# Kernel optimization log

Hardware: AMD Instinct MI355X
Metric: run time of the kernel (lower is better)

Reference implementation:

```python
import jax, jax.numpy as jnp
import numpy as np

B, L, D, H = 8, 1024, 1024, 16
DH = D // H  # dim_per_head = 64
HG = H // 2  # global/local head split


def setup_inputs() -> dict:
    key = jax.random.key(0)
    ks = jax.random.split(key, 10)
    s = 1.0 / np.sqrt(D)
    return {
        "key": jax.random.normal(ks[0], (B, L, D), jnp.float32),
        "value": jax.random.normal(ks[1], (B, L, D), jnp.float32),
        "query": jax.random.normal(ks[2], (B, L, D), jnp.float32),
        "mask": jax.random.bernoulli(ks[3], 0.1, (B, L, L)),
        "additional_mask": jax.random.bernoulli(ks[4], 0.1, (B, L)),
        "Wk": jax.random.normal(ks[5], (D, D), jnp.float32) * s,
        "bk": jnp.zeros((D,), jnp.float32),
        "Wv": jax.random.normal(ks[6], (D, D), jnp.float32) * s,
        "bv": jnp.zeros((D,), jnp.float32),
        "Wq": jax.random.normal(ks[7], (D, D), jnp.float32) * s,
        "bq": jnp.zeros((D,), jnp.float32),
        "Wo": jax.random.normal(ks[8], (D, D), jnp.float32) * s,
        "bo": jnp.zeros((D,), jnp.float32),
    }


def _shape(x):
    # [B, L, D] -> [B, H, L, DH]
    return x.reshape(B, -1, H, DH).transpose(0, 2, 1, 3)


def reference(key, value, query, mask, additional_mask,
              Wk, bk, Wv, bv, Wq, bq, Wo, bo):
    # projections (torch Linear: x @ W.T + b)
    k = _shape(key @ Wk.T + bk)
    v = _shape(value @ Wv.T + bv)
    q = _shape(query @ Wq.T + bq) * (1.0 / np.sqrt(DH))  # scale query (edge_feature=None, additional_mask given)

    qg, ql = q[:, :HG], q[:, HG:]
    kg, kl = k[:, :HG], k[:, HG:]
    vg, vl = v[:, :HG], v[:, HG:]

    # global heads: standard masked attention
    score_g = jnp.einsum('bhqd,bhkd->bhqk', qg, kg)
    top_score = score_g[:, 0]  # taken BEFORE masking, as in original
    score_g = jnp.where(mask[:, None, :, :], -1e18, score_g)
    attn_g = jax.nn.softmax(score_g, axis=-1)  # dropout = identity (eval)
    ctx_g = jnp.einsum('bhqk,bhkd->bhqd', attn_g, vg)

    # local heads: additional_mask [B, k] broadcast over heads and queries
    score_l = jnp.einsum('bhqd,bhkd->bhqk', ql, kl)
    score_l = jnp.where(additional_mask[:, None, None, :], -1e18, score_l)
    attn_l = jax.nn.softmax(score_l, axis=-1)
    ctx_l = jnp.einsum('bhqk,bhkd->bhqd', attn_l, vl)

    ctx = jnp.concatenate([ctx_g, ctx_l], axis=1)          # [B, H, L, DH]
    ctx = ctx.transpose(0, 2, 1, 3).reshape(B, -1, D)      # unshape -> [B, L, D]
    out = ctx @ Wo.T + bo
    return out, top_score
```

## Files before the change

kernel.cpp:

```cpp
#include <hip/hip_runtime.h>
#include <hip/hip_bf16.h>

typedef unsigned short u16;
typedef unsigned int u32;
typedef __attribute__((ext_vector_type(8))) short short8;
typedef __attribute__((ext_vector_type(4))) short short4v;
typedef __attribute__((ext_vector_type(4))) float floatx4;

#define BB 8
#define LL 1024
#define DD 1024
#define HH 16
#define DHH 64
#define NEGBIG (-3.0e38f)
#define QSCALE 0.1803368801111204f
#define LN2F   0.6931471805599453f

__device__ inline u16 f2b(float f) {
  union { __hip_bfloat16 h; u16 u; } cv;
  cv.h = __float2bfloat16(f);
  return cv.u;
}
__device__ inline float b2f(u16 u) {
  union { u16 u; __hip_bfloat16 h; } cv;
  cv.u = u;
  return __bfloat162float(cv.h);
}
__device__ inline float fin(float v, float sentinel) {
  return (fabsf(v) < 1e30f) ? v : sentinel;
}
__device__ inline float fexp2(float x) {
#if __has_builtin(__builtin_amdgcn_exp2f)
  return __builtin_amdgcn_exp2f(x);
#else
  return exp2f(x);
#endif
}
__device__ inline void async16(const void* g, void* l) {
  __builtin_amdgcn_global_load_lds(
      (__attribute__((address_space(1))) void*)(const_cast<void*>(g)),
      (__attribute__((address_space(3))) void*)l, 16, 0, 0);
}


__global__ __launch_bounds__(256) void convpack(
    const float* __restrict__ key, const float* __restrict__ value,
    const float* __restrict__ Wk, const float* __restrict__ Wv,
    const float* __restrict__ Wq, const float* __restrict__ Wo,
    const int* __restrict__ mask, const int* __restrict__ amask,
    u16* __restrict__ keyb, u16* __restrict__ valb, u16* __restrict__ Wkb,
    u16* __restrict__ Wvb, u16* __restrict__ Wqb, u16* __restrict__ Wob,
    u32* __restrict__ maskb, u32* __restrict__ amaskb) {
  const int job = blockIdx.y;
  const int gtid = blockIdx.x * 256 + threadIdx.x;
  const int stride = gridDim.x * 256;

  if (job < 6) {
    const float* src; u16* dst; size_t n4;
    switch (job) {
      case 0: src = key;   dst = keyb; n4 = (size_t)BB * LL * DD / 4; break;
      case 1: src = value; dst = valb; n4 = (size_t)BB * LL * DD / 4; break;
      case 2: src = Wk;    dst = Wkb;  n4 = (size_t)DD * DD / 4; break;
      case 3: src = Wv;    dst = Wvb;  n4 = (size_t)DD * DD / 4; break;
      case 4: src = Wq;    dst = Wqb;  n4 = (size_t)DD * DD / 4; break;
      default: src = Wo;   dst = Wob;  n4 = (size_t)DD * DD / 4; break;
    }
    for (size_t i = gtid; i < n4; i += stride) {
      float4 v = ((const float4*)src)[i];
      short4v s;
      s[0] = (short)f2b(v.x); s[1] = (short)f2b(v.y);
      s[2] = (short)f2b(v.z); s[3] = (short)f2b(v.w);
      *(short4v*)(dst + i * 4) = s;
    }
  } else if (job == 6) {
    const size_t nw = (size_t)BB * LL * LL / 32;
    for (size_t w = gtid; w < nw; w += stride) {
      const int4* src = (const int4*)(mask + w * 32);
      u32 bits = 0;
#pragma unroll
      for (int c = 0; c < 8; c++) {
        int4 v = src[c];
        bits |= (u32)(v.x != 0) << (c * 4);
        bits |= (u32)(v.y != 0) << (c * 4 + 1);
        bits |= (u32)(v.z != 0) << (c * 4 + 2);
        bits |= (u32)(v.w != 0) << (c * 4 + 3);
      }
      maskb[w] = bits;
    }
  } else {
    const int nw = BB * LL / 32;
    for (int w = gtid; w < nw; w += stride) {
      const int4* src = (const int4*)(amask + w * 32);
      u32 bits = 0;
#pragma unroll
      for (int c = 0; c < 8; c++) {
        int4 v = src[c];
        bits |= (u32)(v.x != 0) << (c * 4);
        bits |= (u32)(v.y != 0) << (c * 4 + 1);
        bits |= (u32)(v.z != 0) << (c * 4 + 2);
        bits |= (u32)(v.w != 0) << (c * 4 + 3);
      }
      amaskb[w] = bits;
    }
  }
}

__global__ __launch_bounds__(256) void gemm_qkv(
    const u16* __restrict__ keyb, const u16* __restrict__ valb,
    const float* __restrict__ query, const u16* __restrict__ Wkb,
    const u16* __restrict__ Wvb, const u16* __restrict__ Wqb,
    const float* __restrict__ bk, const float* __restrict__ bv,
    const float* __restrict__ bq, u16* __restrict__ kbuf,
    u16* __restrict__ vbt, u16* __restrict__ qbuf) {
  __shared__ u16 As[128 * 32];
  __shared__ u16 Ws[128 * 32];

  const int z = blockIdx.z;
  const int tid = threadIdx.x;
  const int wave = tid >> 6, lane = tid & 63;
  const int lr = lane & 15, lq = lane >> 4;
  const int row0 = blockIdx.x * 128;
  const int col0 = blockIdx.y * 128;
  const int wm = (wave & 1) * 64, wn = (wave >> 1) * 64;

  floatx4 acc[4][4];
#pragma unroll
  for (int i = 0; i < 4; i++)
#pragma unroll
    for (int j = 0; j < 4; j++) acc[i][j] = (floatx4){0.f, 0.f, 0.f, 0.f};

  const int cc0 = tid, cc1 = 256 + tid;
  u16* As0 = As + wave * 512;
  u16* As1 = As + 2048 + wave * 512;
  u16* Ws0 = Ws + wave * 512;
  u16* Ws1 = Ws + 2048 + wave * 512;

  if (z < 2) {
    const u16* A  = (z == 0) ? keyb : valb;
    const u16* Wb = (z == 0) ? Wkb : Wvb;
    const u16* Ag0 = A + (size_t)(row0 + (cc0 >> 2)) * 1024 + (cc0 & 3) * 8;
    const u16* Ag1 = A + (size_t)(row0 + (cc1 >> 2)) * 1024 + (cc1 & 3) * 8;
    const u16* Wg0 = Wb + (size_t)(col0 + (cc0 >> 2)) * 1024 + (cc0 & 3) * 8;
    const u16* Wg1 = Wb + (size_t)(col0 + (cc1 >> 2)) * 1024 + (cc1 & 3) * 8;

    for (int k0 = 0; k0 < 1024; k0 += 32) {
      __syncthreads();
      async16(Ag0 + k0, As0);
      async16(Ag1 + k0, As1);
      async16(Wg0 + k0, Ws0);
      async16(Wg1 + k0, Ws1);
      __syncthreads();

      short8 af[4], wf[4];
#pragma unroll
      for (int mi = 0; mi < 4; mi++)
        af[mi] = *(const short8*)(As + (wm + mi * 16 + lr) * 32 + lq * 8);
#pragma unroll
      for (int ni = 0; ni < 4; ni++)
        wf[ni] = *(const short8*)(Ws + (wn + ni * 16 + lr) * 32 + lq * 8);
#pragma unroll
      for (int mi = 0; mi < 4; mi++)
#pragma unroll
        for (int ni = 0; ni < 4; ni++)
          acc[mi][ni] = __builtin_amdgcn_mfma_f32_16x16x32_bf16(af[mi], wf[ni],
                                                                acc[mi][ni], 0, 0, 0);
    }
  } else {
    const u16* Wg0 = Wqb + (size_t)(col0 + (cc0 >> 2)) * 1024 + (cc0 & 3) * 8;
    const u16* Wg1 = Wqb + (size_t)(col0 + (cc1 >> 2)) * 1024 + (cc1 & 3) * 8;

    for (int k0 = 0; k0 < 1024; k0 += 32) {
      float4 ag[4];
#pragma unroll
      for (int it = 0; it < 4; it++) {
        const int cc = it * 256 + tid;
        ag[it] = *(const float4*)(query + (size_t)(row0 + (cc >> 3)) * 1024 +
                                  (cc & 7) * 4 + k0);
      }
      __syncthreads();
      async16(Wg0 + k0, Ws0);
      async16(Wg1 + k0, Ws1);
#pragma unroll
      for (int it = 0; it < 4; it++) {
        const int cc = it * 256 + tid;
        short4v s;
        s[0] = (short)f2b(ag[it].x); s[1] = (short)f2b(ag[it].y);
        s[2] = (short)f2b(ag[it].z); s[3] = (short)f2b(ag[it].w);
        *(short4v*)(As + (cc >> 3) * 32 + (cc & 7) * 4) = s;
      }
      __syncthreads();

      short8 af[4], wf[4];
#pragma unroll
      for (int mi = 0; mi < 4; mi++)
        af[mi] = *(const short8*)(As + (wm + mi * 16 + lr) * 32 + lq * 8);
#pragma unroll
      for (int ni = 0; ni < 4; ni++)
        wf[ni] = *(const short8*)(Ws + (wn + ni * 16 + lr) * 32 + lq * 8);
#pragma unroll
      for (int mi = 0; mi < 4; mi++)
#pragma unroll
        for (int ni = 0; ni < 4; ni++)
          acc[mi][ni] = __builtin_amdgcn_mfma_f32_16x16x32_bf16(af[mi], wf[ni],
                                                                acc[mi][ni], 0, 0, 0);
    }
  }

  const float scale = (z == 2) ? QSCALE : 1.0f;
  const float* bias = (z == 0) ? bk : (z == 1) ? bv : bq;
  u16* outb = (z == 0) ? kbuf : qbuf;

#pragma unroll
  for (int ni = 0; ni < 4; ni++) {
    const int col = col0 + wn + ni * 16 + lr;
    const float bvv = bias[col];
#pragma unroll
    for (int mi = 0; mi < 4; mi++) {
#pragma unroll
      for (int r = 0; r < 4; r++) {
        const int row = row0 + wm + mi * 16 + lq * 4 + r;
        const float v = (acc[mi][ni][r] + bvv) * scale;
        const int b = row >> 10, l = row & 1023, h = col >> 6, dh = col & 63;
        if (z == 1)
          vbt[((b * HH + h) * DHH + dh) * LL + l] = f2b(v);
        else
          outb[((b * HH + h) * LL + l) * DHH + dh] = f2b(v);
      }
    }
  }
}

template <int OUT>
__global__ __launch_bounds__(256) void gemm_b(
    const u16* __restrict__ A, const u16* __restrict__ Wb,
    const float* __restrict__ bias, void* __restrict__ outv, float scale) {
  __shared__ u16 As[128 * 32];
  __shared__ u16 Ws[128 * 32];

  const int tid = threadIdx.x;
  const int wave = tid >> 6, lane = tid & 63;
  const int lr = lane & 15, lq = lane >> 4;
  const int row0 = blockIdx.x * 128;
  const int col0 = blockIdx.y * 128;
  const int wm = (wave & 1) * 64, wn = (wave >> 1) * 64;

  floatx4 acc[4][4];
#pragma unroll
  for (int i = 0; i < 4; i++)
#pragma unroll
    for (int j = 0; j < 4; j++) acc[i][j] = (floatx4){0.f, 0.f, 0.f, 0.f};

  const int cc0 = tid, cc1 = 256 + tid;
  const u16* Ag0 = A + (size_t)(row0 + (cc0 >> 2)) * 1024 + (cc0 & 3) * 8;
  const u16* Ag1 = A + (size_t)(row0 + (cc1 >> 2)) * 1024 + (cc1 & 3) * 8;
  const u16* Wg0 = Wb + (size_t)(col0 + (cc0 >> 2)) * 1024 + (cc0 & 3) * 8;
  const u16* Wg1 = Wb + (size_t)(col0 + (cc1 >> 2)) * 1024 + (cc1 & 3) * 8;
  u16* As0 = As + wave * 512;
  u16* As1 = As + 2048 + wave * 512;
  u16* Ws0 = Ws + wave * 512;
  u16* Ws1 = Ws + 2048 + wave * 512;

  for (int k0 = 0; k0 < 1024; k0 += 32) {
    __syncthreads();
    async16(Ag0 + k0, As0);
    async16(Ag1 + k0, As1);
    async16(Wg0 + k0, Ws0);
    async16(Wg1 + k0, Ws1);
    __syncthreads();

    short8 af[4], wf[4];
#pragma unroll
    for (int mi = 0; mi < 4; mi++)
      af[mi] = *(const short8*)(As + (wm + mi * 16 + lr) * 32 + lq * 8);
#pragma unroll
    for (int ni = 0; ni < 4; ni++)
      wf[ni] = *(const short8*)(Ws + (wn + ni * 16 + lr) * 32 + lq * 8);
#pragma unroll
    for (int mi = 0; mi < 4; mi++)
#pragma unroll
      for (int ni = 0; ni < 4; ni++)
        acc[mi][ni] = __builtin_amdgcn_mfma_f32_16x16x32_bf16(af[mi], wf[ni],
                                                              acc[mi][ni], 0, 0, 0);
  }

#pragma unroll
  for (int ni = 0; ni < 4; ni++) {
    const int col = col0 + wn + ni * 16 + lr;
    const float bv = bias[col];
#pragma unroll
    for (int mi = 0; mi < 4; mi++) {
#pragma unroll
      for (int r = 0; r < 4; r++) {
        const int row = row0 + wm + mi * 16 + lq * 4 + r;
        const float v = (acc[mi][ni][r] + bv) * scale;
        if (OUT == 0) {
          const int b = row >> 10, l = row & 1023, h = col >> 6, dh = col & 63;
          ((u16*)outv)[((b * HH + h) * LL + l) * DHH + dh] = f2b(v);
        } else if (OUT == 2) {
          const int b = row >> 10, l = row & 1023, h = col >> 6, dh = col & 63;
          ((u16*)outv)[((b * HH + h) * DHH + dh) * LL + l] = f2b(v);
        } else {
          ((float*)outv)[(size_t)row * 1024 + col] = v;
        }
      }
    }
  }
}

__global__ __launch_bounds__(256) void attn_fast(
    const u16* __restrict__ qbuf, const u16* __restrict__ kbuf,
    const u16* __restrict__ vbt, const u32* __restrict__ maskb,
    const u32* __restrict__ amaskb, u16* __restrict__ ctx,
    float* __restrict__ top) {
  __shared__ u16 Ks[2][64 * 64];
  __shared__ u16 Vts[2][64 * 64];

  const int id = blockIdx.x;
  const int xcd = id & 7;
  const int r_ = id >> 3;
  const int b = r_ & 7;
  const int h = (((r_ >> 3) & 1) << 3) | (xcd ^ b);
  const int qt = r_ >> 4;

  const int tid = threadIdx.x, wave = tid >> 6, lane = tid & 63;
  const int lr = lane & 15, lq = lane >> 4;
  const int lq4 = lq * 4;
  const int x7 = lr & 7;

  const u16* Qg = qbuf + (size_t)((b * HH + h) * LL + qt * 128) * DHH;
  const u16* Kg = kbuf + (size_t)((b * HH + h) * LL) * DHH;
  const u16* Vtg = vbt + (size_t)((b * HH + h) * DHH) * LL;

  short8 qf[2][2];
#pragma unroll
  for (int mi = 0; mi < 2; mi++)
#pragma unroll
    for (int kk = 0; kk < 2; kk++)
      qf[mi][kk] = *(const short8*)(Qg + (wave * 32 + mi * 16 + lr) * 64 +
                                    kk * 32 + lq * 8);

  const int g0 = tid, g1 = 256 + tid;
  const int kr0 = g0 >> 3, kc0 = (g0 & 7) ^ (kr0 & 7);
  const int kr1 = g1 >> 3, kc1 = (g1 & 7) ^ (kr1 & 7);
  const int cs0 = ((0 + lq) ^ x7) * 8;
  const int cs1 = ((4 + lq) ^ x7) * 8;
  const int lqh = lq >> 1, lqb = (lq & 1) * 4;
  const int go00 = ((0 + lqh) ^ x7) * 8 + lqb;
  const int go01 = ((2 + lqh) ^ x7) * 8 + lqb;
  const int go10 = ((4 + lqh) ^ x7) * 8 + lqb;
  const int go11 = ((6 + lqh) ^ x7) * 8 + lqb;

  auto stage = [&](int kc, int buf) {
    async16(Kg + kc * 4096 + kr0 * 64 + kc0 * 8, &Ks[buf][wave * 512]);
    async16(Kg + kc * 4096 + kr1 * 64 + kc1 * 8, &Ks[buf][2048 + wave * 512]);
    async16(Vtg + (size_t)kr0 * LL + kc * 64 + kc0 * 8, &Vts[buf][wave * 512]);
    async16(Vtg + (size_t)kr1 * LL + kc * 64 + kc1 * 8,
            &Vts[buf][2048 + wave * 512]);
  };

  float mrow[2], lrow[2];
  floatx4 Oacc[2][4];
#pragma unroll
  for (int mi = 0; mi < 2; mi++) {
    mrow[mi] = NEGBIG;
    lrow[mi] = 0.f;
#pragma unroll
    for (int ni = 0; ni < 4; ni++) Oacc[mi][ni] = (floatx4){0.f, 0.f, 0.f, 0.f};
  }

  stage(0, 0);

  for (int kc = 0; kc < 16; kc++) {
    const int cur = kc & 1;
    __syncthreads();
    if (kc < 15) stage(kc + 1, cur ^ 1);
    const u16* Ksc = Ks[cur];
    const u16* Vtsc = Vts[cur];

    floatx4 S[2][4];
    __builtin_amdgcn_s_setprio(1);
#pragma unroll
    for (int nj = 0; nj < 4; nj++) {
      const short8 kf0 = *(const short8*)(Ksc + (nj * 16 + lr) * 64 + cs0);
      const short8 kf1 = *(const short8*)(Ksc + (nj * 16 + lr) * 64 + cs1);
#pragma unroll
      for (int mi = 0; mi < 2; mi++) {
        floatx4 z = (floatx4){0.f, 0.f, 0.f, 0.f};
        z = __builtin_amdgcn_mfma_f32_16x16x32_bf16(kf1, qf[mi][1], z, 0, 0, 0);
        z = __builtin_amdgcn_mfma_f32_16x16x32_bf16(kf0, qf[mi][0], z, 0, 0, 0);
        S[mi][nj] = z;
      }
    }
    __builtin_amdgcn_s_setprio(0);

    short8 pf[2][2];
#pragma unroll
    for (int mi = 0; mi < 2; mi++) {
      const int row = qt * 128 + wave * 32 + mi * 16 + lr;

      if (h == 0) {
        float* tp = top + (size_t)(b * LL + row) * LL + kc * 64 + lq4;
#pragma unroll
        for (int nj = 0; nj < 4; nj++) {
          float4 t;
          t.x = S[mi][nj][0] * LN2F; t.y = S[mi][nj][1] * LN2F;
          t.z = S[mi][nj][2] * LN2F; t.w = S[mi][nj][3] * LN2F;
          *(float4*)(tp + nj * 16) = t;
        }
      }

      if (h < 8) {
        const uint2 mw =
            *(const uint2*)(maskb + (size_t)(b * LL + row) * 32 + kc * 2);
#pragma unroll
        for (int nj = 0; nj < 4; nj++) {
          const u32 nib = (((nj & 2) ? mw.y : mw.x) >> ((nj & 1) * 16 + lq4)) & 15u;
#pragma unroll
          for (int r = 0; r < 4; r++)
            if ((nib >> r) & 1) S[mi][nj][r] = -1e18f;
        }
      } else {
        const uint2 aw = *(const uint2*)(amaskb + b * 32 + kc * 2);
#pragma unroll
        for (int nj = 0; nj < 4; nj++) {
          const u32 nib = (((nj & 2) ? aw.y : aw.x) >> ((nj & 1) * 16 + lq4)) & 15u;
#pragma unroll
          for (int r = 0; r < 4; r++)
            if ((nib >> r) & 1) S[mi][nj][r] = -1e18f;
        }
      }

      float cm = fmaxf(fmaxf(S[mi][0][0], S[mi][0][1]),
                       fmaxf(S[mi][0][2], S[mi][0][3]));
#pragma unroll
      for (int nj = 1; nj < 4; nj++)
        cm = fmaxf(cm, fmaxf(fmaxf(S[mi][nj][0], S[mi][nj][1]),
                             fmaxf(S[mi][nj][2], S[mi][nj][3])));
      cm = fmaxf(cm, __shfl_xor(cm, 16, 64));
      cm = fmaxf(cm, __shfl_xor(cm, 32, 64));
      const float mold = mrow[mi];
      const float mnew = fmaxf(mold, cm);
      const float alpha = fexp2(mold - mnew);
      mrow[mi] = mnew;
      float rs = 0.f;
#pragma unroll
      for (int nj = 0; nj < 4; nj++)
#pragma unroll
        for (int r = 0; r < 4; r++) {
          const float p = fexp2(S[mi][nj][r] - mnew);
          S[mi][nj][r] = p;
          rs += p;
        }
      rs += __shfl_xor(rs, 16, 64);
      rs += __shfl_xor(rs, 32, 64);
      lrow[mi] = lrow[mi] * alpha + rs;
#pragma unroll
      for (int ni = 0; ni < 4; ni++)
#pragma unroll
        for (int r = 0; r < 4; r++) Oacc[mi][ni][r] *= alpha;

#pragma unroll
      for (int kk = 0; kk < 2; kk++) {
        short8 p;
#pragma unroll
        for (int r = 0; r < 4; r++) {
          p[r] = (short)f2b(S[mi][2 * kk][r]);
          p[4 + r] = (short)f2b(S[mi][2 * kk + 1][r]);
        }
        pf[mi][kk] = p;
      }
    }

    __builtin_amdgcn_s_setprio(1);
#pragma unroll
    for (int ni = 0; ni < 4; ni++) {
      const int rb = (ni * 16 + lr) * 64;
      const short4v v00 = *(const short4v*)(Vtsc + rb + go00);
      const short4v v01 = *(const short4v*)(Vtsc + rb + go01);
      const short4v v10 = *(const short4v*)(Vtsc + rb + go10);
      const short4v v11 = *(const short4v*)(Vtsc + rb + go11);
      const short8 vf0 = __builtin_shufflevector(v00, v01, 0, 1, 2, 3, 4, 5, 6, 7);
      const short8 vf1 = __builtin_shufflevector(v10, v11, 0, 1, 2, 3, 4, 5, 6, 7);
#pragma unroll
      for (int mi = 0; mi < 2; mi++) {
        Oacc[mi][ni] =
            __builtin_amdgcn_mfma_f32_16x16x32_bf16(vf0, pf[mi][0], Oacc[mi][ni], 0, 0, 0);
        Oacc[mi][ni] =
            __builtin_amdgcn_mfma_f32_16x16x32_bf16(vf1, pf[mi][1], Oacc[mi][ni], 0, 0, 0);
      }
    }
    __builtin_amdgcn_s_setprio(0);
  }

#pragma unroll
  for (int mi = 0; mi < 2; mi++) {
    const float inv = 1.0f / lrow[mi];
    const int row = qt * 128 + wave * 32 + mi * 16 + lr;
    u16* cp = ctx + (size_t)(b * LL + row) * DD + h * DHH + lq4;
#pragma unroll
    for (int ni = 0; ni < 4; ni++) {
      short4v o;
      o[0] = (short)f2b(Oacc[mi][ni][0] * inv);
      o[1] = (short)f2b(Oacc[mi][ni][1] * inv);
      o[2] = (short)f2b(Oacc[mi][ni][2] * inv);
      o[3] = (short)f2b(Oacc[mi][ni][3] * inv);
      *(short4v*)(cp + ni * 16) = o;
    }
  }
}

template <int MODE>
__global__ __launch_bounds__(256) void gemm_k(
    const void* __restrict__ Av, const float* __restrict__ W,
    const float* __restrict__ biasp, void* __restrict__ outv, float scale) {
  __shared__ u16 As[128 * 32];
  __shared__ u16 Ws[128 * 32];
  const int tid = threadIdx.x;
  const int wave = tid >> 6, lane = tid & 63;
  const int lr = lane & 15, lq = lane >> 4;
  const int row0 = blockIdx.x * 128;
  const int col0 = blockIdx.y * 128;
  const int wm = (wave & 1) * 64, wn = (wave >> 1) * 64;
  floatx4 acc[4][4];
#pragma unroll
  for (int i = 0; i < 4; i++)
#pragma unroll
    for (int j = 0; j < 4; j++) acc[i][j] = (floatx4){0.f, 0.f, 0.f, 0.f};
  const float* Af = (const float*)Av;
  const u16* Ab = (const u16*)Av;
  for (int k0 = 0; k0 < 1024; k0 += 32) {
    float4 wg[4];
#pragma unroll
    for (int it = 0; it < 4; it++) {
      const int cc = it * 256 + tid;
      wg[it] = *(const float4*)(W + (size_t)(col0 + (cc >> 3)) * 1024 + (cc & 7) * 4 + k0);
    }
    float4 ag[4];
    short8 ab0, ab1;
    if (MODE == 0) {
#pragma unroll
      for (int it = 0; it < 4; it++) {
        const int cc = it * 256 + tid;
        ag[it] = *(const float4*)(Af + (size_t)(row0 + (cc >> 3)) * 1024 + (cc & 7) * 4 + k0);
      }
    } else {
      const int cc0 = tid, cc1 = 256 + tid;
      ab0 = *(const short8*)(Ab + (size_t)(row0 + (cc0 >> 2)) * 1024 + (cc0 & 3) * 8 + k0);
      ab1 = *(const short8*)(Ab + (size_t)(row0 + (cc1 >> 2)) * 1024 + (cc1 & 3) * 8 + k0);
    }
    __syncthreads();
#pragma unroll
    for (int it = 0; it < 4; it++) {
      const int cc = it * 256 + tid;
      short4v s;
      s[0] = (short)f2b(wg[it].x); s[1] = (short)f2b(wg[it].y);
      s[2] = (short)f2b(wg[it].z); s[3] = (short)f2b(wg[it].w);
      *(short4v*)(Ws + (cc >> 3) * 32 + (cc & 7) * 4) = s;
    }
    if (MODE == 0) {
#pragma unroll
      for (int it = 0; it < 4; it++) {
        const int cc = it * 256 + tid;
        short4v s;
        s[0] = (short)f2b(ag[it].x); s[1] = (short)f2b(ag[it].y);
        s[2] = (short)f2b(ag[it].z); s[3] = (short)f2b(ag[it].w);
        *(short4v*)(As + (cc >> 3) * 32 + (cc & 7) * 4) = s;
      }
    } else {
      *(short8*)(As + tid * 8) = ab0;
      *(short8*)(As + (256 + tid) * 8) = ab1;
    }
    __syncthreads();
    short8 af[4], wf[4];
#pragma unroll
    for (int mi = 0; mi < 4; mi++)
      af[mi] = *(const short8*)(As + (wm + mi * 16 + lr) * 32 + lq * 8);
#pragma unroll
    for (int ni = 0; ni < 4; ni++)
      wf[ni] = *(const short8*)(Ws + (wn + ni * 16 + lr) * 32 + lq * 8);
#pragma unroll
    for (int mi = 0; mi < 4; mi++)
#pragma unroll
      for (int ni = 0; ni < 4; ni++)
        acc[mi][ni] = __builtin_amdgcn_mfma_f32_16x16x32_bf16(af[mi], wf[ni], acc[mi][ni], 0, 0, 0);
  }
#pragma unroll
  for (int ni = 0; ni < 4; ni++) {
    const int col = col0 + wn + ni * 16 + lr;
    const float bv = biasp[col];
#pragma unroll
    for (int mi = 0; mi < 4; mi++) {
#pragma unroll
      for (int r = 0; r < 4; r++) {
        const int row = row0 + wm + mi * 16 + lq * 4 + r;
        float v = (acc[mi][ni][r] + bv) * scale;
        v = fin(v, MODE == 0 ? 700.0f : 1000.0f);
        if (MODE == 0) {
          const int b = row >> 10, l = row & 1023, h = col >> 6, dh = col & 63;
          ((u16*)outv)[((b * HH + h) * LL + l) * DHH + dh] = f2b(v);
        } else {
          ((float*)outv)[(size_t)row * 1024 + col] = v;
        }
      }
    }
  }
}

__global__ __launch_bounds__(256) void attn_kernel(
    const u16* __restrict__ qbuf, const u16* __restrict__ kbuf,
    const u16* __restrict__ vbuf, const int* __restrict__ mask,
    const int* __restrict__ amask, u16* __restrict__ ctx,
    float* __restrict__ top) {
  __shared__ u16 Qs[128 * 64];
  __shared__ u16 Ks[64 * 64];
  __shared__ u16 Vts[64 * 64];
  __shared__ u16 Ps[4][32 * 64];
  const int qt = blockIdx.x, h = blockIdx.y, b = blockIdx.z;
  const int tid = threadIdx.x, wave = tid >> 6, lane = tid & 63;
  const int lr = lane & 15, lq = lane >> 4;
  const u16* Qg = qbuf + (size_t)((b * HH + h) * LL + qt * 128) * DHH;
  const u16* Kg = kbuf + (size_t)((b * HH + h) * LL) * DHH;
  const u16* Vg = vbuf + (size_t)((b * HH + h) * LL) * DHH;
#pragma unroll
  for (int it = 0; it < 4; it++) {
    short8 qv = *(const short8*)(Qg + (it * 256 + tid) * 8);
    *(short8*)(Qs + (it * 256 + tid) * 8) = qv;
  }
  float mrow[2][4], lrow[2][4];
  floatx4 Oacc[2][4];
#pragma unroll
  for (int mi = 0; mi < 2; mi++)
#pragma unroll
    for (int r = 0; r < 4; r++) { mrow[mi][r] = NEGBIG; lrow[mi][r] = 0.f; }
#pragma unroll
  for (int mi = 0; mi < 2; mi++)
#pragma unroll
    for (int ni = 0; ni < 4; ni++) Oacc[mi][ni] = (floatx4){0.f, 0.f, 0.f, 0.f};
  for (int kc = 0; kc < 16; kc++) {
    const u16* Kc = Kg + kc * 64 * DHH;
    const u16* Vc = Vg + kc * 64 * DHH;
    short8 kv0 = *(const short8*)(Kc + tid * 8);
    short8 kv1 = *(const short8*)(Kc + (256 + tid) * 8);
    short8 vv0 = *(const short8*)(Vc + tid * 8);
    short8 vv1 = *(const short8*)(Vc + (256 + tid) * 8);
    __syncthreads();
    *(short8*)(Ks + tid * 8) = kv0;
    *(short8*)(Ks + (256 + tid) * 8) = kv1;
    {
      const int r0 = tid >> 3, e0 = (tid & 7) * 8;
#pragma unroll
      for (int j = 0; j < 8; j++) Vts[(e0 + j) * 64 + r0] = (u16)vv0[j];
      const int cc1 = 256 + tid;
      const int r1 = cc1 >> 3, e1 = (cc1 & 7) * 8;
#pragma unroll
      for (int j = 0; j < 8; j++) Vts[(e1 + j) * 64 + r1] = (u16)vv1[j];
    }
    __syncthreads();
    floatx4 S[2][4];
    short8 qf[2][2];
#pragma unroll
    for (int mi = 0; mi < 2; mi++)
#pragma unroll
      for (int kk = 0; kk < 2; kk++)
        qf[mi][kk] = *(const short8*)(Qs + (wave * 32 + mi * 16 + lr) * 64 + kk * 32 + lq * 8);
#pragma unroll
    for (int nj = 0; nj < 4; nj++) {
      short8 kf0 = *(const short8*)(Ks + (nj * 16 + lr) * 64 + lq * 8);
      short8 kf1 = *(const short8*)(Ks + (nj * 16 + lr) * 64 + 32 + lq * 8);
#pragma unroll
      for (int mi = 0; mi < 2; mi++) {
        floatx4 z = (floatx4){0.f, 0.f, 0.f, 0.f};
        z = __builtin_amdgcn_mfma_f32_16x16x32_bf16(qf[mi][1], kf1, z, 0, 0, 0);
        z = __builtin_amdgcn_mfma_f32_16x16x32_bf16(qf[mi][0], kf0, z, 0, 0, 0);
        S[mi][nj] = z;
      }
    }
#pragma unroll
    for (int mi = 0; mi < 2; mi++)
#pragma unroll
      for (int nj = 0; nj < 4; nj++)
#pragma unroll
        for (int r = 0; r < 4; r++) S[mi][nj][r] = fin(S[mi][nj][r], 800.0f);
    if (h == 0) {
#pragma unroll
      for (int mi = 0; mi < 2; mi++)
#pragma unroll
        for (int nj = 0; nj < 4; nj++)
#pragma unroll
          for (int r = 0; r < 4; r++) {
            const int row = qt * 128 + wave * 32 + mi * 16 + lq * 4 + r;
            const int colk = kc * 64 + nj * 16 + lr;
            top[(size_t)(b * LL + row) * LL + colk] = S[mi][nj][r];
          }
    }
    if (h < 8) {
#pragma unroll
      for (int mi = 0; mi < 2; mi++)
#pragma unroll
        for (int r = 0; r < 4; r++) {
          const int row = qt * 128 + wave * 32 + mi * 16 + lq * 4 + r;
          const int* mp = mask + (size_t)(b * LL + row) * LL + kc * 64;
#pragma unroll
          for (int nj = 0; nj < 4; nj++) {
            const int mv = mp[nj * 16 + lr];
            S[mi][nj][r] = mv ? -1e18f : S[mi][nj][r];
          }
        }
    } else {
#pragma unroll
      for (int nj = 0; nj < 4; nj++) {
        const int mv = amask[b * LL + kc * 64 + nj * 16 + lr];
        if (mv) {
#pragma unroll
          for (int mi = 0; mi < 2; mi++)
#pragma unroll
            for (int r = 0; r < 4; r++) S[mi][nj][r] = -1e18f;
        }
      }
    }
#pragma unroll
    for (int mi = 0; mi < 2; mi++) {
#pragma unroll
      for (int r = 0; r < 4; r++) {
        float cm = S[mi][0][r];
#pragma unroll
        for (int nj = 1; nj < 4; nj++) cm = fmaxf(cm, S[mi][nj][r]);
#pragma unroll
        for (int off = 1; off < 16; off <<= 1) cm = fmaxf(cm, __shfl_xor(cm, off, 64));
        const float mold = mrow[mi][r];
        const float mnew = fmaxf(mold, cm);
        const float alpha = __expf(mold - mnew);
        mrow[mi][r] = mnew;
        float rs = 0.f;
#pragma unroll
        for (int nj = 0; nj < 4; nj++) {
          const float p = __expf(S[mi][nj][r] - mnew);
          S[mi][nj][r] = p;
          rs += p;
        }
#pragma unroll
        for (int off = 1; off < 16; off <<= 1) rs += __shfl_xor(rs, off, 64);
        lrow[mi][r] = lrow[mi][r] * alpha + rs;
#pragma unroll
        for (int ni = 0; ni < 4; ni++) Oacc[mi][ni][r] *= alpha;
      }
    }
#pragma unroll
    for (int mi = 0; mi < 2; mi++)
#pragma unroll
      for (int nj = 0; nj < 4; nj++)
#pragma unroll
        for (int r = 0; r < 4; r++)
          Ps[wave][(mi * 16 + lq * 4 + r) * 64 + nj * 16 + lr] = f2b(S[mi][nj][r]);
    __syncthreads();
#pragma unroll
    for (int kk = 0; kk < 2; kk++) {
      short8 pf[2];
#pragma unroll
      for (int mi = 0; mi < 2; mi++)
        pf[mi] = *(const short8*)(&Ps[wave][(mi * 16 + lr) * 64 + kk * 32 + lq * 8]);
#pragma unroll
      for (int ni = 0; ni < 4; ni++) {
        short8 vf = *(const short8*)(Vts + (ni * 16 + lr) * 64 + kk * 32 + lq * 8);
#pragma unroll
        for (int mi = 0; mi < 2; mi++)
          Oacc[mi][ni] = __builtin_amdgcn_mfma_f32_16x16x32_bf16(pf[mi], vf, Oacc[mi][ni], 0, 0, 0);
      }
    }
  }
#pragma unroll
  for (int mi = 0; mi < 2; mi++)
#pragma unroll
    for (int r = 0; r < 4; r++) {
      const float inv = 1.0f / lrow[mi][r];
      const int row = qt * 128 + wave * 32 + mi * 16 + lq * 4 + r;
#pragma unroll
      for (int ni = 0; ni < 4; ni++) {
        const int col = h * DHH + ni * 16 + lr;
        ctx[(size_t)(b * LL + row) * DD + col] = f2b(fin(Oacc[mi][ni][r] * inv, 900.0f));
      }
    }
}

extern "C" void kernel_launch(void* const* d_in, const int* in_sizes, int n_in,
                              void* d_out, int out_size, void* d_ws, size_t ws_size,
                              hipStream_t stream) {
  const float* key   = (const float*)d_in[0];
  const float* value = (const float*)d_in[1];
  const float* query = (const float*)d_in[2];
  const int* mask    = (const int*)d_in[3];
  const int* amask   = (const int*)d_in[4];
  const float* Wk = (const float*)d_in[5];
  const float* bk = (const float*)d_in[6];
  const float* Wv = (const float*)d_in[7];
  const float* bv = (const float*)d_in[8];
  const float* Wq = (const float*)d_in[9];
  const float* bq = (const float*)d_in[10];
  const float* Wo = (const float*)d_in[11];
  const float* bo = (const float*)d_in[12];

  float* outp = (float*)d_out;
  float* topp = outp + (size_t)BB * LL * DD;

  const size_t M8 = (size_t)BB * LL * DD;
  const size_t M1 = (size_t)DD * DD;
  const size_t NEED = (size_t)90 * 1024 * 1024;

  dim3 tb(256), gg(64, 8, 1), ga(8, 16, 8);

  if (ws_size >= NEED) {
    u16* W16 = (u16*)d_ws;
    u16* keyb = W16;
    u16* valb = W16 + M8;
    u16* qbuf = W16 + 2 * M8;
    u16* Wkb = W16 + 3 * M8;
    u16* Wvb = Wkb + M1;
    u16* Wqb = Wvb + M1;
    u16* Wob = Wqb + M1;
    u32* maskb = (u32*)(Wob + M1);
    u32* amaskb = maskb + 262144;
    u16* kbuf = W16 + 3 * M8 + 5 * M1;
    u16* vbt  = kbuf + M8;
    u16* cbuf = valb;

    convpack<<<dim3(256, 8), tb, 0, stream>>>(
        key, value, Wk, Wv, Wq, Wo, mask, amask,
        keyb, valb, Wkb, Wvb, Wqb, Wob, maskb, amaskb);
    gemm_qkv<<<dim3(64, 8, 3), tb, 0, stream>>>(
        keyb, valb, query, Wkb, Wvb, Wqb, bk, bv, bq, kbuf, vbt, qbuf);
    attn_fast<<<dim3(1024, 1, 1), tb, 0, stream>>>(qbuf, kbuf, vbt, maskb,
                                                   amaskb, cbuf, topp);
    gemm_b<1><<<gg, tb, 0, stream>>>(cbuf, Wob, bo, outp, 1.0f);
  } else {
    u16* kbuf = (u16*)d_ws;
    u16* vbuf = kbuf + M8;
    u16* qbuf = vbuf + M8;
    u16* cbuf = qbuf + M8;
    gemm_k<0><<<gg, tb, 0, stream>>>(key,   Wk, bk, kbuf, 1.0f);
    gemm_k<0><<<gg, tb, 0, stream>>>(value, Wv, bv, vbuf, 1.0f);
    gemm_k<0><<<gg, tb, 0, stream>>>(query, Wq, bq, qbuf, 0.125f);
    attn_kernel<<<ga, tb, 0, stream>>>(qbuf, kbuf, vbuf, mask, amask, cbuf, topp);
    gemm_k<1><<<gg, tb, 0, stream>>>(cbuf, Wo, bo, outp, 1.0f);
  }
}
```

Baseline: 428.4 us.

## Double-buffer LDS tiles in projection GEMMs to overlap global loads with MFMA

Converts the QKV and output projection GEMMs from single-buffered LDS tiles with two barriers per k-step to double-buffered tiles. The next tiles are prefetched asynchronously with explicit vmcnt waits, or through registers for the fp32 query path, while MFMAs run on the current buffer. This is meant to hide global-load latency behind compute. In exchange it doubles LDS use per block, which may reduce occupancy, and it relies on correct manual waitcnt accounting.

New measurement: 434.2 us. Within noise of the previous version (+1.3%).

```diff
diff --git a/kernel.cpp b/kernel.cpp
--- a/kernel.cpp
+++ b/kernel.cpp
@@ -112,8 +112,8 @@
     const float* __restrict__ bk, const float* __restrict__ bv,
     const float* __restrict__ bq, u16* __restrict__ kbuf,
     u16* __restrict__ vbt, u16* __restrict__ qbuf) {
-  __shared__ u16 As[128 * 32];
-  __shared__ u16 Ws[128 * 32];
+  __shared__ u16 As[2][128 * 32];
+  __shared__ u16 Ws[2][128 * 32];
 
   const int z = blockIdx.z;
   const int tid = threadIdx.x;
@@ -130,10 +130,6 @@
     for (int j = 0; j < 4; j++) acc[i][j] = (floatx4){0.f, 0.f, 0.f, 0.f};
 
   const int cc0 = tid, cc1 = 256 + tid;
-  u16* As0 = As + wave * 512;
-  u16* As1 = As + 2048 + wave * 512;
-  u16* Ws0 = Ws + wave * 512;
-  u16* Ws1 = Ws + 2048 + wave * 512;
 
   if (z < 2) {
     const u16* A  = (z == 0) ? keyb : valb;
@@ -143,66 +139,101 @@
     const u16* Wg0 = Wb + (size_t)(col0 + (cc0 >> 2)) * 1024 + (cc0 & 3) * 8;
     const u16* Wg1 = Wb + (size_t)(col0 + (cc1 >> 2)) * 1024 + (cc1 & 3) * 8;
 
-    for (int k0 = 0; k0 < 1024; k0 += 32) {
-      __syncthreads();
-      async16(Ag0 + k0, As0);
-      async16(Ag1 + k0, As1);
-      async16(Wg0 + k0, Ws0);
-      async16(Wg1 + k0, Ws1);
-      __syncthreads();
+    auto stage = [&](int t, int buf) {
+      const int o = t * 32;
+      async16(Ag0 + o, &As[buf][wave * 512]);
+      async16(Ag1 + o, &As[buf][2048 + wave * 512]);
+      async16(Wg0 + o, &Ws[buf][wave * 512]);
+      async16(Wg1 + o, &Ws[buf][2048 + wave * 512]);
+    };
+
+    stage(0, 0);
+    stage(1, 1);
+
+    for (int t = 0; t < 32; t++) {
+      const int buf = t & 1;
+      if (t < 31) asm volatile("s_waitcnt vmcnt(4)" ::: "memory");
+      else        asm volatile("s_waitcnt vmcnt(0)" ::: "memory");
+      __builtin_amdgcn_s_barrier();
+      __builtin_amdgcn_sched_barrier(0);
 
       short8 af[4], wf[4];
 #pragma unroll
       for (int mi = 0; mi < 4; mi++)
-        af[mi] = *(const short8*)(As + (wm + mi * 16 + lr) * 32 + lq * 8);
+        af[mi] = *(const short8*)(&As[buf][(wm + mi * 16 + lr) * 32 + lq * 8]);
 #pragma unroll
       for (int ni = 0; ni < 4; ni++)
-        wf[ni] = *(const short8*)(Ws + (wn + ni * 16 + lr) * 32 + lq * 8);
+        wf[ni] = *(const short8*)(&Ws[buf][(wn + ni * 16 + lr) * 32 + lq * 8]);
 #pragma unroll
       for (int mi = 0; mi < 4; mi++)
 #pragma unroll
         for (int ni = 0; ni < 4; ni++)
           acc[mi][ni] = __builtin_amdgcn_mfma_f32_16x16x32_bf16(af[mi], wf[ni],
                                                                 acc[mi][ni], 0, 0, 0);
+
+      __builtin_amdgcn_sched_barrier(0);
+      __builtin_amdgcn_s_barrier();
+      if (t < 30) stage(t + 2, buf);
     }
   } else {
     const u16* Wg0 = Wqb + (size_t)(col0 + (cc0 >> 2)) * 1024 + (cc0 & 3) * 8;
     const u16* Wg1 = Wqb + (size_t)(col0 + (cc1 >> 2)) * 1024 + (cc1 & 3) * 8;
 
-    for (int k0 = 0; k0 < 1024; k0 += 32) {
-      float4 ag[4];
+    auto stageW = [&](int t, int buf) {
+      const int o = t * 32;
+      async16(Wg0 + o, &Ws[buf][wave * 512]);
+      async16(Wg1 + o, &Ws[buf][2048 + wave * 512]);
+    };
+    auto loadA = [&](int t, float4* ag) {
 #pragma unroll
       for (int it = 0; it < 4; it++) {
         const int cc = it * 256 + tid;
         ag[it] = *(const float4*)(query + (size_t)(row0 + (cc >> 3)) * 1024 +
-                                  (cc & 7) * 4 + k0);
-      }
-      __syncthreads();
-      async16(Wg0 + k0, Ws0);
-      async16(Wg1 + k0, Ws1);
+                                  (cc & 7) * 4 + t * 32);
+      }
+    };
+    auto writeA = [&](int buf, const float4* ag) {
 #pragma unroll
       for (int it = 0; it < 4; it++) {
         const int cc = it * 256 + tid;
         short4v s;
         s[0] = (short)f2b(ag[it].x); s[1] = (short)f2b(ag[it].y);
         s[2] = (short)f2b(ag[it].z); s[3] = (short)f2b(ag[it].w);
-        *(short4v*)(As + (cc >> 3) * 32 + (cc & 7) * 4) = s;
-      }
+        *(short4v*)(&As[buf][(cc >> 3) * 32 + (cc & 7) * 4]) = s;
+      }
+    };
+
+    {
+      float4 ag0[4];
+      loadA(0, ag0);
+      stageW(0, 0);
+      writeA(0, ag0);
+    }
+
+    for (int t = 0; t < 32; t++) {
+      const int buf = t & 1;
       __syncthreads();
+      float4 ag[4];
+      if (t < 31) {
+        stageW(t + 1, buf ^ 1);
+        loadA(t + 1, ag);
+      }
 
       short8 af[4], wf[4];
 #pragma unroll
       for (int mi = 0; mi < 4; mi++)
-        af[mi] = *(const short8*)(As + (wm + mi * 16 + lr) * 32 + lq * 8);
+        af[mi] = *(const short8*)(&As[buf][(wm + mi * 16 + lr) * 32 + lq * 8]);
 #pragma unroll
       for (int ni = 0; ni < 4; ni++)
-        wf[ni] = *(const short8*)(Ws + (wn + ni * 16 + lr) * 32 + lq * 8);
+        wf[ni] = *(const short8*)(&Ws[buf][(wn + ni * 16 + lr) * 32 + lq * 8]);
 #pragma unroll
       for (int mi = 0; mi < 4; mi++)
 #pragma unroll
         for (int ni = 0; ni < 4; ni++)
           acc[mi][ni] = __builtin_amdgcn_mfma_f32_16x16x32_bf16(af[mi], wf[ni],
                                                                 acc[mi][ni], 0, 0, 0);
+
+      if (t < 31) writeA(buf ^ 1, ag);
     }
   }
 
@@ -234,8 +265,8 @@
 __global__ __launch_bounds__(256) void gemm_b(
     const u16* __restrict__ A, const u16* __restrict__ Wb,
     const float* __restrict__ bias, void* __restrict__ outv, float scale) {
-  __shared__ u16 As[128 * 32];
-  __shared__ u16 Ws[128 * 32];
+  __shared__ u16 As[2][128 * 32];
+  __shared__ u16 Ws[2][128 * 32];
 
   const int tid = threadIdx.x;
   const int wave = tid >> 6, lane = tid & 63;
@@ -255,32 +286,42 @@
   const u16* Ag1 = A + (size_t)(row0 + (cc1 >> 2)) * 1024 + (cc1 & 3) * 8;
   const u16* Wg0 = Wb + (size_t)(col0 + (cc0 >> 2)) * 1024 + (cc0 & 3) * 8;
   const u16* Wg1 = Wb + (size_t)(col0 + (cc1 >> 2)) * 1024 + (cc1 & 3) * 8;
-  u16* As0 = As + wave * 512;
-  u16* As1 = As + 2048 + wave * 512;
-  u16* Ws0 = Ws + wave * 512;
-  u16* Ws1 = Ws + 2048 + wave * 512;
-
-  for (int k0 = 0; k0 < 1024; k0 += 32) {
-    __syncthreads();
-    async16(Ag0 + k0, As0);
-    async16(Ag1 + k0, As1);
-    async16(Wg0 + k0, Ws0);
-    async16(Wg1 + k0, Ws1);
-    __syncthreads();
+
+  auto stage = [&](int t, int buf) {
+    const int o = t * 32;
+    async16(Ag0 + o, &As[buf][wave * 512]);
+    async16(Ag1 + o, &As[buf][2048 + wave * 512]);
+    async16(Wg0 + o, &Ws[buf][wave * 512]);
+    async16(Wg1 + o, &Ws[buf][2048 + wave * 512]);
+  };
+
+  stage(0, 0);
+  stage(1, 1);
+
+  for (int t = 0; t < 32; t++) {
+    const int buf = t & 1;
+    if (t < 31) asm volatile("s_waitcnt vmcnt(4)" ::: "memory");
+    else        asm volatile("s_waitcnt vmcnt(0)" ::: "memory");
+    __builtin_amdgcn_s_barrier();
+    __builtin_amdgcn_sched_barrier(0);
 
     short8 af[4], wf[4];
 #pragma unroll
     for (int mi = 0; mi < 4; mi++)
-      af[mi] = *(const short8*)(As + (wm + mi * 16 + lr) * 32 + lq * 8);
+      af[mi] = *(const short8*)(&As[buf][(wm + mi * 16 + lr) * 32 + lq * 8]);
 #pragma unroll
     for (int ni = 0; ni < 4; ni++)
-      wf[ni] = *(const short8*)(Ws + (wn + ni * 16 + lr) * 32 + lq * 8);
+      wf[ni] = *(const short8*)(&Ws[buf][(wn + ni * 16 + lr) * 32 + lq * 8]);
 #pragma unroll
     for (int mi = 0; mi < 4; mi++)
 #pragma unroll
       for (int ni = 0; ni < 4; ni++)
         acc[mi][ni] = __builtin_amdgcn_mfma_f32_16x16x32_bf16(af[mi], wf[ni],
                                                               acc[mi][ni], 0, 0, 0);
+
+    __builtin_amdgcn_sched_barrier(0);
+    __builtin_amdgcn_s_barrier();
+    if (t < 30) stage(t + 2, buf);
   }
 
 #pragma unroll
```
